# Kernel optimization log

Measured on AMD Instinct MI355X. Metric: run time of the kernel, lower is better.

The kernel has to match this reference:

```python
import jax, jax.numpy as jnp
import numpy as np

D_OUT = 1024

def setup_inputs() -> dict:
    key = jax.random.key(0)
    k1, k2, k3, k4 = jax.random.split(key, 4)
    x = jax.random.normal(k1, (4, 2048, 1024), dtype=jnp.float32)
    # torch.nn.Linear weights are [d_out, d_in]
    s = 1.0 / np.sqrt(1024)
    W_q = jax.random.uniform(k2, (D_OUT, 1024), dtype=jnp.float32, minval=-s, maxval=s)
    W_k = jax.random.uniform(k3, (D_OUT, 1024), dtype=jnp.float32, minval=-s, maxval=s)
    W_v = jax.random.uniform(k4, (D_OUT, 1024), dtype=jnp.float32, minval=-s, maxval=s)
    return {"x": x, "W_q": W_q, "W_k": W_k, "W_v": W_v}

def reference(x, W_q, W_k, W_v):
    b, n, d_in = x.shape
    q = jnp.einsum('bnd,od->bno', x, W_q)  # [b, n, d_out]
    k = jnp.einsum('bnd,od->bno', x, W_k)
    v = jnp.einsum('bnd,od->bno', x, W_v)
    scores = jnp.einsum('bqd,bkd->bqk', q, k)  # full N x N score matrix
    causal = jnp.tril(jnp.ones((n, n), dtype=bool))
    scores = jnp.where(causal, scores, -jnp.inf)
    weights = jax.nn.softmax(scores / jnp.sqrt(jnp.float32(D_OUT)), axis=-1)
    # dropout p=0.0 -> identity (eval)
    return jnp.einsum('bqk,bkd->bqd', weights, v)
```

## Files before the change

kernel.cpp:

```cpp
#include <hip/hip_runtime.h>
#include <hip/hip_bf16.h>
#include <stdint.h>
#include <math.h>

typedef unsigned short ushort_t;
typedef __attribute__((ext_vector_type(4))) float f32x4;
typedef __attribute__((ext_vector_type(8))) __bf16 bf16x8;
typedef __attribute__((ext_vector_type(8))) unsigned short ushort8;
typedef __attribute__((ext_vector_type(4))) unsigned short ushort4v;

__device__ __forceinline__ float bf2f(ushort_t u) {
  union { unsigned u32; float f; } x; x.u32 = ((unsigned)u) << 16; return x.f;
}
__device__ __forceinline__ ushort_t f2bf(float f) {
  union { float f; unsigned u; } x; x.f = f;
  unsigned r = x.u + 0x7FFF + ((x.u >> 16) & 1);
  return (ushort_t)(r >> 16);
}

__device__ __forceinline__ void gld16(const ushort_t* g, ushort_t* l) {
  __builtin_amdgcn_global_load_lds(
      (const __attribute__((address_space(1))) uint32_t*)g,
      (__attribute__((address_space(3))) uint32_t*)l, 16, 0, 0);
}

__global__ __launch_bounds__(256) void cast_all_kernel(
    const float* __restrict__ x, const float* __restrict__ wq,
    const float* __restrict__ wk, const float* __restrict__ wv,
    ushort_t* __restrict__ xb, ushort_t* __restrict__ wqb,
    ushort_t* __restrict__ wkb, ushort_t* __restrict__ wvb,
    float* __restrict__ rowsum) {
  int blk = blockIdx.x;
  if (blk >= 4096 + 1536) {
    int idx = (blk - (4096 + 1536)) * 256 + threadIdx.x;
    f32x4 z = {0.f, 0.f, 0.f, 0.f};
    ((f32x4*)rowsum)[idx * 2] = z;
    ((f32x4*)rowsum)[idx * 2 + 1] = z;
    return;
  }
  const float* in;
  ushort_t* out;
  int i;
  if (blk < 4096) {
    in = x; out = xb; i = blk * 256 + threadIdx.x;
  } else {
    int w = (blk - 4096) >> 9;
    int lb = (blk - 4096) & 511;
    in = (w == 0) ? wq : (w == 1) ? wk : wv;
    out = (w == 0) ? wqb : (w == 1) ? wkb : wvb;
    i = lb * 256 + threadIdx.x;
  }
  const f32x4* p = (const f32x4*)in;
  f32x4 a = p[2 * i];
  f32x4 b = p[2 * i + 1];
  ushort8 o;
  o[0] = f2bf(a[0]); o[1] = f2bf(a[1]); o[2] = f2bf(a[2]); o[3] = f2bf(a[3]);
  o[4] = f2bf(b[0]); o[5] = f2bf(b[1]); o[6] = f2bf(b[2]); o[7] = f2bf(b[3]);
  *((ushort8*)out + i) = o;
}

#define BM 128
#define BN 128
#define BK 64

__device__ __forceinline__ void gemm_core(
    const ushort_t* __restrict__ A, const ushort_t* __restrict__ B, int Kd,
    int kEnd, int m0, int n0, ushort_t* As, ushort_t* Bs, f32x4 (&acc)[4][4]) {
  int tid = threadIdx.x;
  int lane = tid & 63;
  int wave = tid >> 6;
  int wr = (wave >> 1) * 64;
  int wc = (wave & 1) * 64;
  int ln15 = lane & 15;
  int kq = lane >> 4;

  int row = tid >> 3;
  int ksw = ((tid & 7) ^ (row & 7)) * 8;
  const ushort_t* aB = A + (size_t)(m0 + row) * Kd + ksw;
  const ushort_t* bB = B + (size_t)(n0 + row) * Kd + ksw;
  int xk = ln15 & 7;

  for (int k0 = 0; k0 < kEnd; k0 += BK) {
    __syncthreads();
#pragma unroll
    for (int r = 0; r < 4; ++r) {
      gld16(aB + (size_t)(32 * r) * Kd + k0, &As[(tid + 256 * r) * 8]);
      gld16(bB + (size_t)(32 * r) * Kd + k0, &Bs[(tid + 256 * r) * 8]);
    }
    __syncthreads();
#pragma unroll
    for (int s = 0; s < 2; ++s) {
      bf16x8 af[4], bfr[4];
#pragma unroll
      for (int i = 0; i < 4; ++i)
        af[i] = *(const bf16x8*)
            &As[(wr + i * 16 + ln15) * BK + (((s * 4 + kq) ^ xk) * 8)];
#pragma unroll
      for (int j = 0; j < 4; ++j)
        bfr[j] = *(const bf16x8*)
            &Bs[(wc + j * 16 + ln15) * BK + (((s * 4 + kq) ^ xk) * 8)];
#pragma unroll
      for (int i = 0; i < 4; ++i)
#pragma unroll
        for (int j = 0; j < 4; ++j)
          acc[i][j] = __builtin_amdgcn_mfma_f32_16x16x32_bf16(
              af[i], bfr[j], acc[i][j], 0, 0, 0);
    }
  }
}

__global__ __launch_bounds__(256, 4) void gemm_s(
    const ushort_t* __restrict__ Qg, const ushort_t* __restrict__ Kg,
    ushort_t* __restrict__ Eg, float scale, float* __restrict__ rowsum) {
  int t = blockIdx.x;
  int m = (int)((sqrtf(8.f * (float)t + 1.f) - 1.f) * 0.5f);
  while ((m + 1) * (m + 2) / 2 <= t) ++m;
  while (m * (m + 1) / 2 > t) --m;
  int n = t - m * (m + 1) / 2;
  int m0 = m * BM, n0 = n * BN;
  int bz = blockIdx.z;
  const ushort_t* A = Qg + (size_t)bz * (2048 * 1024);
  const ushort_t* B = Kg + (size_t)bz * (2048 * 1024);

  __shared__ ushort_t As[BM * BK];
  __shared__ ushort_t Bs[BN * BK];

  f32x4 acc[4][4];
#pragma unroll
  for (int i = 0; i < 4; ++i)
#pragma unroll
    for (int j = 0; j < 4; ++j) acc[i][j] = f32x4{0.f, 0.f, 0.f, 0.f};

  gemm_core(A, B, 1024, 1024, m0, n0, As, Bs, acc);

  int tid = threadIdx.x;
  int lane = tid & 63;
  int wave = tid >> 6;
  int wr = (wave >> 1) * 64;
  int wc = (wave & 1) * 64;
  int ln15 = lane & 15;
  int kq = lane >> 4;

  ushort_t* C = Eg + (size_t)bz * (2048 * 2048);
  float* rs = rowsum + (size_t)bz * 2048;
#pragma unroll
  for (int i = 0; i < 4; ++i) {
    int row0 = m0 + wr + i * 16 + kq * 4;
#pragma unroll
    for (int r = 0; r < 4; ++r) {
      int grow = row0 + r;
      float psum = 0.f;
#pragma unroll
      for (int j = 0; j < 4; ++j) {
        int col = n0 + wc + j * 16 + ln15;
        float e = (col <= grow) ? __expf(acc[i][j][r] * scale) : 0.f;
        C[(size_t)grow * 2048 + col] = f2bf(e);
        psum += e;
      }
      psum += __shfl_xor(psum, 1);
      psum += __shfl_xor(psum, 2);
      psum += __shfl_xor(psum, 4);
      psum += __shfl_xor(psum, 8);
      if (ln15 == 0) atomicAdd(&rs[grow], psum);
    }
  }
}

__global__ __launch_bounds__(256, 4) void gemm_o(
    const ushort_t* __restrict__ Eg, const ushort_t* __restrict__ Vg,
    float* __restrict__ Og, const float* __restrict__ rowsum) {
  int m = (blockIdx.z < 2) ? (int)(gridDim.x - 1 - blockIdx.x)
                           : (int)blockIdx.x;
  int m0 = m * BM, n0 = blockIdx.y * BN;
  int kEnd = min(2048, m0 + BM);
  int bz = blockIdx.z;
  const ushort_t* A = Eg + (size_t)bz * (2048 * 2048);
  const ushort_t* B = Vg + (size_t)bz * (1024 * 2048);

  __shared__ ushort_t As[BM * BK];
  __shared__ ushort_t Bs[BN * BK];

  f32x4 acc[4][4];
#pragma unroll
  for (int i = 0; i < 4; ++i)
#pragma unroll
    for (int j = 0; j < 4; ++j) acc[i][j] = f32x4{0.f, 0.f, 0.f, 0.f};

  gemm_core(A, B, 2048, kEnd, m0, n0, As, Bs, acc);

  int tid = threadIdx.x;
  int lane = tid & 63;
  int wave = tid >> 6;
  int wr = (wave >> 1) * 64;
  int wc = (wave & 1) * 64;
  int ln15 = lane & 15;
  int kq = lane >> 4;

  float* C = Og + (size_t)bz * (2048 * 1024);
  const float* rs = rowsum + (size_t)bz * 2048;
#pragma unroll
  for (int i = 0; i < 4; ++i) {
    int row0 = m0 + wr + i * 16 + kq * 4;
#pragma unroll
    for (int r = 0; r < 4; ++r) {
      float inv = 1.0f / rs[row0 + r];
#pragma unroll
      for (int j = 0; j < 4; ++j) {
        int col = n0 + wc + j * 16 + ln15;
        C[(size_t)(row0 + r) * 1024 + col] = acc[i][j][r] * inv;
      }
    }
  }
}

__global__ __launch_bounds__(256, 4) void gemm_qkv(
    const ushort_t* __restrict__ xb, const ushort_t* __restrict__ wq,
    const ushort_t* __restrict__ wk, const ushort_t* __restrict__ wv,
    ushort_t* __restrict__ Qb, ushort_t* __restrict__ Kb,
    ushort_t* __restrict__ Vt) {
  int m0 = blockIdx.x * BM, n0 = blockIdx.y * BN;
  int z = blockIdx.z;
  const ushort_t* B = (z == 0) ? wq : (z == 1) ? wk : wv;

  __shared__ ushort_t As[BM * BK];
  __shared__ ushort_t Bs[BN * BK];

  f32x4 acc[4][4];
#pragma unroll
  for (int i = 0; i < 4; ++i)
#pragma unroll
    for (int j = 0; j < 4; ++j) acc[i][j] = f32x4{0.f, 0.f, 0.f, 0.f};

  gemm_core(xb, B, 1024, 1024, m0, n0, As, Bs, acc);

  int tid = threadIdx.x;
  int lane = tid & 63;
  int wave = tid >> 6;
  int wr = (wave >> 1) * 64;
  int wc = (wave & 1) * 64;
  int ln15 = lane & 15;
  int kq = lane >> 4;

  if (z < 2) {
    ushort_t* C = (z == 0) ? Qb : Kb;
#pragma unroll
    for (int i = 0; i < 4; ++i) {
      int row0 = m0 + wr + i * 16 + kq * 4;
#pragma unroll
      for (int j = 0; j < 4; ++j) {
        int col = n0 + wc + j * 16 + ln15;
#pragma unroll
        for (int r = 0; r < 4; ++r)
          C[(size_t)(row0 + r) * 1024 + col] = f2bf(acc[i][j][r]);
      }
    }
  } else {
#pragma unroll
    for (int i = 0; i < 4; ++i) {
      int gm = m0 + wr + i * 16 + kq * 4;
      int b = gm >> 11, nn = gm & 2047;
#pragma unroll
      for (int j = 0; j < 4; ++j) {
        int d = n0 + wc + j * 16 + ln15;
        ushort4v v;
#pragma unroll
        for (int r = 0; r < 4; ++r) v[r] = f2bf(acc[i][j][r]);
        *(ushort4v*)&Vt[(size_t)b * (2048 * 1024) + (size_t)d * 2048 + nn] = v;
      }
    }
  }
}

extern "C" void kernel_launch(void* const* d_in, const int* in_sizes, int n_in,
                              void* d_out, int out_size, void* d_ws, size_t ws_size,
                              hipStream_t stream) {
  const float* x = (const float*)d_in[0];
  const float* Wq = (const float*)d_in[1];
  const float* Wk = (const float*)d_in[2];
  const float* Wv = (const float*)d_in[3];
  float* out = (float*)d_out;
  char* ws = (char*)d_ws;

  ushort_t* xb = (ushort_t*)(ws);
  ushort_t* wqb = (ushort_t*)(ws + (16ull << 20));
  ushort_t* wkb = (ushort_t*)(ws + (18ull << 20));
  ushort_t* wvb = (ushort_t*)(ws + (20ull << 20));
  ushort_t* Qb = (ushort_t*)(ws + (22ull << 20));
  ushort_t* Kb = (ushort_t*)(ws + (38ull << 20));
  ushort_t* Vt = (ushort_t*)(ws + (54ull << 20));
  ushort_t* Eb = (ushort_t*)(ws + (70ull << 20));
  float* rowsum = (float*)(ws + (102ull << 20));

  cast_all_kernel<<<4096 + 3 * 512 + 4, 256, 0, stream>>>(
      x, Wq, Wk, Wv, xb, wqb, wkb, wvb, rowsum);

  dim3 gQKV(8192 / BM, 1024 / BN, 3);
  gemm_qkv<<<gQKV, 256, 0, stream>>>(xb, wqb, wkb, wvb, Qb, Kb, Vt);

  dim3 gS(136, 1, 4);
  gemm_s<<<gS, 256, 0, stream>>>(Qb, Kb, Eb, 0.03125f, rowsum);

  dim3 gO(2048 / BM, 1024 / BN, 4);
  gemm_o<<<gO, 256, 0, stream>>>(Eb, Vt, out, rowsum);
}
```

Measured before the change: 224.1 us.

## Rewrite QKV GEMM as 256x256 tile, 8-wave, double-buffered phased pipeline

Replaces the QKV projection GEMM with a 512-thread kernel that computes 256x256 output tiles. It uses double-buffered LDS and interleaves global-to-LDS loads across eight phases with explicit waitcnt, barriers and raised MFMA priority. The goal is to overlap memory traffic with MFMA work and cut global loads per flop through a larger tile. The launch-bounds occupancy hint for gemm_s and gemm_o also drops from 4 to 3 blocks, giving those kernels more registers at the cost of occupancy. The larger tile leaves only 384 blocks and needs 128 KB of LDS per block, and the hand-written vmcnt accounting is fragile.

```diff
diff --git a/kernel.cpp b/kernel.cpp
--- a/kernel.cpp
+++ b/kernel.cpp
@@ -109,7 +109,7 @@
   }
 }
 
-__global__ __launch_bounds__(256, 4) void gemm_s(
+__global__ __launch_bounds__(256, 3) void gemm_s(
     const ushort_t* __restrict__ Qg, const ushort_t* __restrict__ Kg,
     ushort_t* __restrict__ Eg, float scale, float* __restrict__ rowsum) {
   int t = blockIdx.x;
@@ -166,7 +166,7 @@
   }
 }
 
-__global__ __launch_bounds__(256, 4) void gemm_o(
+__global__ __launch_bounds__(256, 3) void gemm_o(
     const ushort_t* __restrict__ Eg, const ushort_t* __restrict__ Vg,
     float* __restrict__ Og, const float* __restrict__ rowsum) {
   int m = (blockIdx.z < 2) ? (int)(gridDim.x - 1 - blockIdx.x)
@@ -213,58 +213,118 @@
   }
 }
 
-__global__ __launch_bounds__(256, 4) void gemm_qkv(
+#define STA(BUF, T, Q) \
+  gld16(aS + (size_t)((Q) * 64) * 1024 + (T) * 64, &As[BUF][(Q)*4096 + tid * 8])
+#define STB(BUF, T, R) \
+  gld16(bS + (size_t)((R) * 64) * 1024 + (T) * 64, &Bs[BUF][(R)*4096 + tid * 8])
+
+#define PHASE(BUF, MH, KS, STAGES, TAIL) do {                               \
+    bf16x8 af[4], bfv[4];                                                   \
+    _Pragma("unroll")                                                       \
+    for (int f = 0; f < 4; ++f)                                             \
+      af[f] = *(const bf16x8*)&As[BUF][                                     \
+          (wm * 128 + (MH) * 64 + f * 16 + ln15) * 64 +                     \
+          ((((KS) * 4 + kq) ^ xk) * 8)];                                    \
+    _Pragma("unroll")                                                       \
+    for (int n = 0; n < 4; ++n)                                             \
+      bfv[n] = *(const bf16x8*)&Bs[BUF][                                    \
+          (wn * 64 + n * 16 + ln15) * 64 + ((((KS) * 4 + kq) ^ xk) * 8)];   \
+    STAGES;                                                                 \
+    asm volatile("s_waitcnt lgkmcnt(0)" ::: "memory");                      \
+    __builtin_amdgcn_sched_barrier(0);                                      \
+    __builtin_amdgcn_s_setprio(1);                                          \
+    _Pragma("unroll")                                                       \
+    for (int f = 0; f < 4; ++f)                                             \
+      _Pragma("unroll")                                                     \
+      for (int n = 0; n < 4; ++n)                                           \
+        acc[(MH) * 4 + f][n] = __builtin_amdgcn_mfma_f32_16x16x32_bf16(     \
+            af[f], bfv[n], acc[(MH) * 4 + f][n], 0, 0, 0);                  \
+    __builtin_amdgcn_s_setprio(0);                                          \
+    TAIL;                                                                   \
+    __builtin_amdgcn_sched_barrier(0);                                      \
+    __builtin_amdgcn_s_barrier();                                           \
+    __builtin_amdgcn_sched_barrier(0);                                      \
+  } while (0)
+
+__global__ __launch_bounds__(512, 2) void gemm_qkv8p(
     const ushort_t* __restrict__ xb, const ushort_t* __restrict__ wq,
     const ushort_t* __restrict__ wk, const ushort_t* __restrict__ wv,
     ushort_t* __restrict__ Qb, ushort_t* __restrict__ Kb,
     ushort_t* __restrict__ Vt) {
-  int m0 = blockIdx.x * BM, n0 = blockIdx.y * BN;
+  int m0 = blockIdx.x * 256, n0 = blockIdx.y * 256;
   int z = blockIdx.z;
-  const ushort_t* B = (z == 0) ? wq : (z == 1) ? wk : wv;
-
-  __shared__ ushort_t As[BM * BK];
-  __shared__ ushort_t Bs[BN * BK];
-
-  f32x4 acc[4][4];
-#pragma unroll
-  for (int i = 0; i < 4; ++i)
-#pragma unroll
-    for (int j = 0; j < 4; ++j) acc[i][j] = f32x4{0.f, 0.f, 0.f, 0.f};
-
-  gemm_core(xb, B, 1024, 1024, m0, n0, As, Bs, acc);
+  const ushort_t* Bw = (z == 0) ? wq : (z == 1) ? wk : wv;
+  const int nt = 16;
+
+  __shared__ ushort_t As[2][256 * 64];
+  __shared__ ushort_t Bs[2][256 * 64];
 
   int tid = threadIdx.x;
   int lane = tid & 63;
   int wave = tid >> 6;
-  int wr = (wave >> 1) * 64;
-  int wc = (wave & 1) * 64;
-  int ln15 = lane & 15;
-  int kq = lane >> 4;
+  int wm = wave >> 2, wn = wave & 3;
+  int ln15 = lane & 15, kq = lane >> 4, xk = ln15 & 7;
+
+  const ushort_t* aS = xb + (size_t)(m0 + (tid >> 3)) * 1024 +
+                       (((tid & 7) ^ ((tid >> 3) & 7)) * 8);
+  const ushort_t* bS = Bw + (size_t)(n0 + (tid >> 3)) * 1024 +
+                       (((tid & 7) ^ ((tid >> 3) & 7)) * 8);
+
+  f32x4 acc[8][4];
+#pragma unroll
+  for (int a = 0; a < 8; ++a)
+#pragma unroll
+    for (int n = 0; n < 4; ++n) acc[a][n] = f32x4{0.f, 0.f, 0.f, 0.f};
+
+  STA(0, 0, 0); STA(0, 0, 1); STA(0, 0, 2); STA(0, 0, 3);
+  STB(0, 0, 0); STB(0, 0, 1); STB(0, 0, 2); STB(0, 0, 3);
+  STA(1, 1, 0); STA(1, 1, 2);
+  asm volatile("s_waitcnt vmcnt(2)" ::: "memory");
+  __builtin_amdgcn_sched_barrier(0);
+  __builtin_amdgcn_s_barrier();
+  __builtin_amdgcn_sched_barrier(0);
+
+  for (int i = 0; i < nt / 2; ++i) {
+    int t0 = 2 * i, t1 = 2 * i + 1;
+    bool s2 = (t0 + 2) < nt, s3 = (t1 + 2) < nt;
+    PHASE(0, 0, 0,
+          { STA(1, t1, 1); STA(1, t1, 3); STB(1, t1, 0); STB(1, t1, 1); }, );
+    PHASE(0, 0, 1, { STB(1, t1, 2); STB(1, t1, 3); }, );
+    PHASE(0, 1, 0, { if (s2) { STA(0, t0 + 2, 0); STA(0, t0 + 2, 2); } }, );
+    PHASE(0, 1, 1, , {
+      if (s2) { asm volatile("s_waitcnt vmcnt(2)" ::: "memory"); }
+      else    { asm volatile("s_waitcnt vmcnt(0)" ::: "memory"); } });
+    PHASE(1, 0, 0, { if (s2) { STA(0, t0 + 2, 1); STA(0, t0 + 2, 3); } }, );
+    PHASE(1, 0, 1, { if (s2) { STB(0, t0 + 2, 0); STB(0, t0 + 2, 1); } }, );
+    PHASE(1, 1, 0, { if (s2) { STB(0, t0 + 2, 2); STB(0, t0 + 2, 3); } }, );
+    PHASE(1, 1, 1, { if (s3) { STA(1, t1 + 2, 0); STA(1, t1 + 2, 2); } },
+          { asm volatile("s_waitcnt vmcnt(2)" ::: "memory"); });
+  }
 
   if (z < 2) {
     ushort_t* C = (z == 0) ? Qb : Kb;
 #pragma unroll
-    for (int i = 0; i < 4; ++i) {
-      int row0 = m0 + wr + i * 16 + kq * 4;
-#pragma unroll
-      for (int j = 0; j < 4; ++j) {
-        int col = n0 + wc + j * 16 + ln15;
+    for (int a = 0; a < 8; ++a) {
+      int row0 = m0 + wm * 128 + (a >> 2) * 64 + (a & 3) * 16 + kq * 4;
+#pragma unroll
+      for (int n = 0; n < 4; ++n) {
+        int col = n0 + wn * 64 + n * 16 + ln15;
 #pragma unroll
         for (int r = 0; r < 4; ++r)
-          C[(size_t)(row0 + r) * 1024 + col] = f2bf(acc[i][j][r]);
+          C[(size_t)(row0 + r) * 1024 + col] = f2bf(acc[a][n][r]);
       }
     }
   } else {
 #pragma unroll
-    for (int i = 0; i < 4; ++i) {
-      int gm = m0 + wr + i * 16 + kq * 4;
+    for (int a = 0; a < 8; ++a) {
+      int gm = m0 + wm * 128 + (a >> 2) * 64 + (a & 3) * 16 + kq * 4;
       int b = gm >> 11, nn = gm & 2047;
 #pragma unroll
-      for (int j = 0; j < 4; ++j) {
-        int d = n0 + wc + j * 16 + ln15;
+      for (int n = 0; n < 4; ++n) {
+        int d = n0 + wn * 64 + n * 16 + ln15;
         ushort4v v;
 #pragma unroll
-        for (int r = 0; r < 4; ++r) v[r] = f2bf(acc[i][j][r]);
+        for (int r = 0; r < 4; ++r) v[r] = f2bf(acc[a][n][r]);
         *(ushort4v*)&Vt[(size_t)b * (2048 * 1024) + (size_t)d * 2048 + nn] = v;
       }
     }
@@ -294,8 +354,8 @@
   cast_all_kernel<<<4096 + 3 * 512 + 4, 256, 0, stream>>>(
       x, Wq, Wk, Wv, xb, wqb, wkb, wvb, rowsum);
 
-  dim3 gQKV(8192 / BM, 1024 / BN, 3);
-  gemm_qkv<<<gQKV, 256, 0, stream>>>(xb, wqb, wkb, wvb, Qb, Kb, Vt);
+  dim3 gQKV(8192 / 256, 1024 / 256, 3);
+  gemm_qkv8p<<<gQKV, 512, 0, stream>>>(xb, wqb, wkb, wvb, Qb, Kb, Vt);
 
   dim3 gS(136, 1, 4);
   gemm_s<<<gS, 256, 0, stream>>>(Qb, Kb, Eb, 0.03125f, rowsum);
```

Measured after the change: 239.0 us. +6.6%, slower.

## Move V projection into the score kernel launch to balance work

Applied to the files above, without the earlier changes.

The QKV projection kernel now computes only Q and K. The V projection tiles are appended to the causal score kernel's grid, so one launch handles both the triangular S tiles and the V GEMM tiles. The aim is to fill the idle tail of the triangular score grid with independent V work, while the QK launch shrinks. Launch bounds are also lowered from 4 to 3 blocks per CU, which permits more registers per thread but lowers occupancy.

```diff
diff --git a/kernel.cpp b/kernel.cpp
--- a/kernel.cpp
+++ b/kernel.cpp
@@ -109,18 +109,13 @@
   }
 }
 
-__global__ __launch_bounds__(256, 4) void gemm_s(
-    const ushort_t* __restrict__ Qg, const ushort_t* __restrict__ Kg,
-    ushort_t* __restrict__ Eg, float scale, float* __restrict__ rowsum) {
-  int t = blockIdx.x;
-  int m = (int)((sqrtf(8.f * (float)t + 1.f) - 1.f) * 0.5f);
-  while ((m + 1) * (m + 2) / 2 <= t) ++m;
-  while (m * (m + 1) / 2 > t) --m;
-  int n = t - m * (m + 1) / 2;
-  int m0 = m * BM, n0 = n * BN;
-  int bz = blockIdx.z;
-  const ushort_t* A = Qg + (size_t)bz * (2048 * 1024);
-  const ushort_t* B = Kg + (size_t)bz * (2048 * 1024);
+__global__ __launch_bounds__(256, 3) void gemm_qk(
+    const ushort_t* __restrict__ xb, const ushort_t* __restrict__ wq,
+    const ushort_t* __restrict__ wk, ushort_t* __restrict__ Qb,
+    ushort_t* __restrict__ Kb) {
+  int m0 = blockIdx.x * BM, n0 = blockIdx.y * BN;
+  int z = blockIdx.z;
+  const ushort_t* B = (z == 0) ? wq : wk;
 
   __shared__ ushort_t As[BM * BK];
   __shared__ ushort_t Bs[BN * BK];
@@ -131,7 +126,7 @@
 #pragma unroll
     for (int j = 0; j < 4; ++j) acc[i][j] = f32x4{0.f, 0.f, 0.f, 0.f};
 
-  gemm_core(A, B, 1024, 1024, m0, n0, As, Bs, acc);
+  gemm_core(xb, B, 1024, 1024, m0, n0, As, Bs, acc);
 
   int tid = threadIdx.x;
   int lane = tid & 63;
@@ -141,32 +136,108 @@
   int ln15 = lane & 15;
   int kq = lane >> 4;
 
-  ushort_t* C = Eg + (size_t)bz * (2048 * 2048);
-  float* rs = rowsum + (size_t)bz * 2048;
+  ushort_t* C = (z == 0) ? Qb : Kb;
 #pragma unroll
   for (int i = 0; i < 4; ++i) {
     int row0 = m0 + wr + i * 16 + kq * 4;
 #pragma unroll
-    for (int r = 0; r < 4; ++r) {
-      int grow = row0 + r;
-      float psum = 0.f;
+    for (int j = 0; j < 4; ++j) {
+      int col = n0 + wc + j * 16 + ln15;
+#pragma unroll
+      for (int r = 0; r < 4; ++r)
+        C[(size_t)(row0 + r) * 1024 + col] = f2bf(acc[i][j][r]);
+    }
+  }
+}
+
+__global__ __launch_bounds__(256, 3) void gemm_sv(
+    const ushort_t* __restrict__ Qg, const ushort_t* __restrict__ Kg,
+    const ushort_t* __restrict__ xb, const ushort_t* __restrict__ wv,
+    ushort_t* __restrict__ Eg, ushort_t* __restrict__ Vt,
+    float scale, float* __restrict__ rowsum) {
+  int bx = blockIdx.x;
+  int bz = blockIdx.z;
+  bool isS = bx < 136;
+  int m0, n0;
+  const ushort_t *A, *B;
+  if (isS) {
+    int t = bx;
+    int m = (int)((sqrtf(8.f * (float)t + 1.f) - 1.f) * 0.5f);
+    while ((m + 1) * (m + 2) / 2 <= t) ++m;
+    while (m * (m + 1) / 2 > t) --m;
+    int n = t - m * (m + 1) / 2;
+    m0 = m * BM; n0 = n * BN;
+    A = Qg + (size_t)bz * (2048 * 1024);
+    B = Kg + (size_t)bz * (2048 * 1024);
+  } else {
+    int vid = (bx - 136) + 128 * bz;
+    m0 = (vid >> 3) * BM;
+    n0 = (vid & 7) * BN;
+    A = xb;
+    B = wv;
+  }
+
+  __shared__ ushort_t As[BM * BK];
+  __shared__ ushort_t Bs[BN * BK];
+
+  f32x4 acc[4][4];
+#pragma unroll
+  for (int i = 0; i < 4; ++i)
+#pragma unroll
+    for (int j = 0; j < 4; ++j) acc[i][j] = f32x4{0.f, 0.f, 0.f, 0.f};
+
+  gemm_core(A, B, 1024, 1024, m0, n0, As, Bs, acc);
+
+  int tid = threadIdx.x;
+  int lane = tid & 63;
+  int wave = tid >> 6;
+  int wr = (wave >> 1) * 64;
+  int wc = (wave & 1) * 64;
+  int ln15 = lane & 15;
+  int kq = lane >> 4;
+
+  if (isS) {
+    ushort_t* C = Eg + (size_t)bz * (2048 * 2048);
+    float* rs = rowsum + (size_t)bz * 2048;
+#pragma unroll
+    for (int i = 0; i < 4; ++i) {
+      int row0 = m0 + wr + i * 16 + kq * 4;
+#pragma unroll
+      for (int r = 0; r < 4; ++r) {
+        int grow = row0 + r;
+        float psum = 0.f;
+#pragma unroll
+        for (int j = 0; j < 4; ++j) {
+          int col = n0 + wc + j * 16 + ln15;
+          float e = (col <= grow) ? __expf(acc[i][j][r] * scale) : 0.f;
+          C[(size_t)grow * 2048 + col] = f2bf(e);
+          psum += e;
+        }
+        psum += __shfl_xor(psum, 1);
+        psum += __shfl_xor(psum, 2);
+        psum += __shfl_xor(psum, 4);
+        psum += __shfl_xor(psum, 8);
+        if (ln15 == 0) atomicAdd(&rs[grow], psum);
+      }
+    }
+  } else {
+#pragma unroll
+    for (int i = 0; i < 4; ++i) {
+      int gm = m0 + wr + i * 16 + kq * 4;
+      int b = gm >> 11, nn = gm & 2047;
 #pragma unroll
       for (int j = 0; j < 4; ++j) {
-        int col = n0 + wc + j * 16 + ln15;
-        float e = (col <= grow) ? __expf(acc[i][j][r] * scale) : 0.f;
-        C[(size_t)grow * 2048 + col] = f2bf(e);
-        psum += e;
+        int d = n0 + wc + j * 16 + ln15;
+        ushort4v v;
+#pragma unroll
+        for (int r = 0; r < 4; ++r) v[r] = f2bf(acc[i][j][r]);
+        *(ushort4v*)&Vt[(size_t)b * (2048 * 1024) + (size_t)d * 2048 + nn] = v;
       }
-      psum += __shfl_xor(psum, 1);
-      psum += __shfl_xor(psum, 2);
-      psum += __shfl_xor(psum, 4);
-      psum += __shfl_xor(psum, 8);
-      if (ln15 == 0) atomicAdd(&rs[grow], psum);
-    }
-  }
-}
-
-__global__ __launch_bounds__(256, 4) void gemm_o(
+    }
+  }
+}
+
+__global__ __launch_bounds__(256, 3) void gemm_o(
     const ushort_t* __restrict__ Eg, const ushort_t* __restrict__ Vg,
     float* __restrict__ Og, const float* __restrict__ rowsum) {
   int m = (blockIdx.z < 2) ? (int)(gridDim.x - 1 - blockIdx.x)
@@ -213,64 +284,6 @@
   }
 }
 
-__global__ __launch_bounds__(256, 4) void gemm_qkv(
-    const ushort_t* __restrict__ xb, const ushort_t* __restrict__ wq,
-    const ushort_t* __restrict__ wk, const ushort_t* __restrict__ wv,
-    ushort_t* __restrict__ Qb, ushort_t* __restrict__ Kb,
-    ushort_t* __restrict__ Vt) {
-  int m0 = blockIdx.x * BM, n0 = blockIdx.y * BN;
-  int z = blockIdx.z;
-  const ushort_t* B = (z == 0) ? wq : (z == 1) ? wk : wv;
-
-  __shared__ ushort_t As[BM * BK];
-  __shared__ ushort_t Bs[BN * BK];
-
-  f32x4 acc[4][4];
-#pragma unroll
-  for (int i = 0; i < 4; ++i)
-#pragma unroll
-    for (int j = 0; j < 4; ++j) acc[i][j] = f32x4{0.f, 0.f, 0.f, 0.f};
-
-  gemm_core(xb, B, 1024, 1024, m0, n0, As, Bs, acc);
-
-  int tid = threadIdx.x;
-  int lane = tid & 63;
-  int wave = tid >> 6;
-  int wr = (wave >> 1) * 64;
-  int wc = (wave & 1) * 64;
-  int ln15 = lane & 15;
-  int kq = lane >> 4;
-
-  if (z < 2) {
-    ushort_t* C = (z == 0) ? Qb : Kb;
-#pragma unroll
-    for (int i = 0; i < 4; ++i) {
-      int row0 = m0 + wr + i * 16 + kq * 4;
-#pragma unroll
-      for (int j = 0; j < 4; ++j) {
-        int col = n0 + wc + j * 16 + ln15;
-#pragma unroll
-        for (int r = 0; r < 4; ++r)
-          C[(size_t)(row0 + r) * 1024 + col] = f2bf(acc[i][j][r]);
-      }
-    }
-  } else {
-#pragma unroll
-    for (int i = 0; i < 4; ++i) {
-      int gm = m0 + wr + i * 16 + kq * 4;
-      int b = gm >> 11, nn = gm & 2047;
-#pragma unroll
-      for (int j = 0; j < 4; ++j) {
-        int d = n0 + wc + j * 16 + ln15;
-        ushort4v v;
-#pragma unroll
-        for (int r = 0; r < 4; ++r) v[r] = f2bf(acc[i][j][r]);
-        *(ushort4v*)&Vt[(size_t)b * (2048 * 1024) + (size_t)d * 2048 + nn] = v;
-      }
-    }
-  }
-}
-
 extern "C" void kernel_launch(void* const* d_in, const int* in_sizes, int n_in,
                               void* d_out, int out_size, void* d_ws, size_t ws_size,
                               hipStream_t stream) {
@@ -294,11 +307,11 @@
   cast_all_kernel<<<4096 + 3 * 512 + 4, 256, 0, stream>>>(
       x, Wq, Wk, Wv, xb, wqb, wkb, wvb, rowsum);
 
-  dim3 gQKV(8192 / BM, 1024 / BN, 3);
-  gemm_qkv<<<gQKV, 256, 0, stream>>>(xb, wqb, wkb, wvb, Qb, Kb, Vt);
-
-  dim3 gS(136, 1, 4);
-  gemm_s<<<gS, 256, 0, stream>>>(Qb, Kb, Eb, 0.03125f, rowsum);
+  dim3 gQK(8192 / BM, 1024 / BN, 2);
+  gemm_qk<<<gQK, 256, 0, stream>>>(xb, wqb, wkb, Qb, Kb);
+
+  dim3 gSV(136 + 128, 1, 4);
+  gemm_sv<<<gSV, 256, 0, stream>>>(Qb, Kb, xb, wvb, Eb, Vt, 0.03125f, rowsum);
 
   dim3 gO(2048 / BM, 1024 / BN, 4);
   gemm_o<<<gO, 256, 0, stream>>>(Eb, Vt, out, rowsum);
```

Result: no change. 222.9 us (-0.6%).

## Remap GEMM block indices to XCDs so each batch stays in one L2

Applied to the files above, without the earlier changes.

Flattens all three GEMM grids to 1D and decodes the block index so blocks dispatched round-robin to the same XCD work on the same batch (two XCDs per batch), keeping Q/K/V/E reuse inside one XCD's L2. The causal score tiles are split between the XCD pair with a balancing rule, and the output GEMM interleaves long and short row-tiles. Launch bounds also drop from 4 to 3 waves per SIMD. This relies on the hardware's round-robin dispatch order across XCDs, and the serial tile-search loop in gemm_s adds a little per-block overhead.

```diff
diff --git a/kernel.cpp b/kernel.cpp
--- a/kernel.cpp
+++ b/kernel.cpp
@@ -109,18 +109,22 @@
   }
 }
 
-__global__ __launch_bounds__(256, 4) void gemm_s(
-    const ushort_t* __restrict__ Qg, const ushort_t* __restrict__ Kg,
-    ushort_t* __restrict__ Eg, float scale, float* __restrict__ rowsum) {
-  int t = blockIdx.x;
-  int m = (int)((sqrtf(8.f * (float)t + 1.f) - 1.f) * 0.5f);
-  while ((m + 1) * (m + 2) / 2 <= t) ++m;
-  while (m * (m + 1) / 2 > t) --m;
-  int n = t - m * (m + 1) / 2;
-  int m0 = m * BM, n0 = n * BN;
-  int bz = blockIdx.z;
-  const ushort_t* A = Qg + (size_t)bz * (2048 * 1024);
-  const ushort_t* B = Kg + (size_t)bz * (2048 * 1024);
+__global__ __launch_bounds__(256, 3) void gemm_qkv(
+    const ushort_t* __restrict__ xb, const ushort_t* __restrict__ wq,
+    const ushort_t* __restrict__ wk, const ushort_t* __restrict__ wv,
+    ushort_t* __restrict__ Qb, ushort_t* __restrict__ Kb,
+    ushort_t* __restrict__ Vt) {
+  int L = blockIdx.x;
+  int xcd = L & 7;
+  int slot = L >> 3;
+  int bz = xcd >> 1, p = xcd & 1;
+  int zz = slot >> 6;
+  int tt = slot & 63;
+  int m_local = ((tt >> 3) << 1) + p;
+  int n = tt & 7;
+  int m0 = (bz * 16 + m_local) * BM;
+  int n0 = n * BN;
+  const ushort_t* B = (zz == 0) ? wq : (zz == 1) ? wk : wv;
 
   __shared__ ushort_t As[BM * BK];
   __shared__ ushort_t Bs[BN * BK];
@@ -131,7 +135,7 @@
 #pragma unroll
     for (int j = 0; j < 4; ++j) acc[i][j] = f32x4{0.f, 0.f, 0.f, 0.f};
 
-  gemm_core(A, B, 1024, 1024, m0, n0, As, Bs, acc);
+  gemm_core(xb, B, 1024, 1024, m0, n0, As, Bs, acc);
 
   int tid = threadIdx.x;
   int lane = tid & 63;
@@ -141,41 +145,55 @@
   int ln15 = lane & 15;
   int kq = lane >> 4;
 
-  ushort_t* C = Eg + (size_t)bz * (2048 * 2048);
-  float* rs = rowsum + (size_t)bz * 2048;
-#pragma unroll
-  for (int i = 0; i < 4; ++i) {
-    int row0 = m0 + wr + i * 16 + kq * 4;
-#pragma unroll
-    for (int r = 0; r < 4; ++r) {
-      int grow = row0 + r;
-      float psum = 0.f;
+  if (zz < 2) {
+    ushort_t* C = (zz == 0) ? Qb : Kb;
+#pragma unroll
+    for (int i = 0; i < 4; ++i) {
+      int row0 = m0 + wr + i * 16 + kq * 4;
 #pragma unroll
       for (int j = 0; j < 4; ++j) {
         int col = n0 + wc + j * 16 + ln15;
-        float e = (col <= grow) ? __expf(acc[i][j][r] * scale) : 0.f;
-        C[(size_t)grow * 2048 + col] = f2bf(e);
-        psum += e;
-      }
-      psum += __shfl_xor(psum, 1);
-      psum += __shfl_xor(psum, 2);
-      psum += __shfl_xor(psum, 4);
-      psum += __shfl_xor(psum, 8);
-      if (ln15 == 0) atomicAdd(&rs[grow], psum);
-    }
-  }
-}
-
-__global__ __launch_bounds__(256, 4) void gemm_o(
-    const ushort_t* __restrict__ Eg, const ushort_t* __restrict__ Vg,
-    float* __restrict__ Og, const float* __restrict__ rowsum) {
-  int m = (blockIdx.z < 2) ? (int)(gridDim.x - 1 - blockIdx.x)
-                           : (int)blockIdx.x;
-  int m0 = m * BM, n0 = blockIdx.y * BN;
-  int kEnd = min(2048, m0 + BM);
-  int bz = blockIdx.z;
-  const ushort_t* A = Eg + (size_t)bz * (2048 * 2048);
-  const ushort_t* B = Vg + (size_t)bz * (1024 * 2048);
+#pragma unroll
+        for (int r = 0; r < 4; ++r)
+          C[(size_t)(row0 + r) * 1024 + col] = f2bf(acc[i][j][r]);
+      }
+    }
+  } else {
+#pragma unroll
+    for (int i = 0; i < 4; ++i) {
+      int gm = m0 + wr + i * 16 + kq * 4;
+      int b = gm >> 11, nn = gm & 2047;
+#pragma unroll
+      for (int j = 0; j < 4; ++j) {
+        int d = n0 + wc + j * 16 + ln15;
+        ushort4v v;
+#pragma unroll
+        for (int r = 0; r < 4; ++r) v[r] = f2bf(acc[i][j][r]);
+        *(ushort4v*)&Vt[(size_t)b * (2048 * 1024) + (size_t)d * 2048 + nn] = v;
+      }
+    }
+  }
+}
+
+__global__ __launch_bounds__(256, 3) void gemm_s(
+    const ushort_t* __restrict__ Qg, const ushort_t* __restrict__ Kg,
+    ushort_t* __restrict__ Eg, float scale, float* __restrict__ rowsum) {
+  int L = blockIdx.x;
+  int xcd = L & 7;
+  int slot = L >> 3;
+  int bz = xcd >> 1, p = xcd & 1;
+  int t = slot, m = 16, n = 0;
+  for (int mi = 0; mi < 16 && m == 16; ++mi)
+    for (int ni = 0; ni <= mi; ++ni) {
+      int assignOdd = (ni & 1) || ((ni == mi) && !(ni & 1) && (mi >= 8));
+      if (assignOdd == p) {
+        if (t == 0) { m = mi; n = ni; break; }
+        --t;
+      }
+    }
+  int m0 = m * BM, n0 = n * BN;
+  const ushort_t* A = Qg + (size_t)bz * (2048 * 1024);
+  const ushort_t* B = Kg + (size_t)bz * (2048 * 1024);
 
   __shared__ ushort_t As[BM * BK];
   __shared__ ushort_t Bs[BN * BK];
@@ -186,7 +204,7 @@
 #pragma unroll
     for (int j = 0; j < 4; ++j) acc[i][j] = f32x4{0.f, 0.f, 0.f, 0.f};
 
-  gemm_core(A, B, 2048, kEnd, m0, n0, As, Bs, acc);
+  gemm_core(A, B, 1024, 1024, m0, n0, As, Bs, acc);
 
   int tid = threadIdx.x;
   int lane = tid & 63;
@@ -196,31 +214,46 @@
   int ln15 = lane & 15;
   int kq = lane >> 4;
 
-  float* C = Og + (size_t)bz * (2048 * 1024);
-  const float* rs = rowsum + (size_t)bz * 2048;
+  ushort_t* C = Eg + (size_t)bz * (2048 * 2048);
+  float* rs = rowsum + (size_t)bz * 2048;
 #pragma unroll
   for (int i = 0; i < 4; ++i) {
     int row0 = m0 + wr + i * 16 + kq * 4;
 #pragma unroll
     for (int r = 0; r < 4; ++r) {
-      float inv = 1.0f / rs[row0 + r];
+      int grow = row0 + r;
+      float psum = 0.f;
 #pragma unroll
       for (int j = 0; j < 4; ++j) {
         int col = n0 + wc + j * 16 + ln15;
-        C[(size_t)(row0 + r) * 1024 + col] = acc[i][j][r] * inv;
-      }
-    }
-  }
-}
-
-__global__ __launch_bounds__(256, 4) void gemm_qkv(
-    const ushort_t* __restrict__ xb, const ushort_t* __restrict__ wq,
-    const ushort_t* __restrict__ wk, const ushort_t* __restrict__ wv,
-    ushort_t* __restrict__ Qb, ushort_t* __restrict__ Kb,
-    ushort_t* __restrict__ Vt) {
-  int m0 = blockIdx.x * BM, n0 = blockIdx.y * BN;
-  int z = blockIdx.z;
-  const ushort_t* B = (z == 0) ? wq : (z == 1) ? wk : wv;
+        float e = (col <= grow) ? __expf(acc[i][j][r] * scale) : 0.f;
+        C[(size_t)grow * 2048 + col] = f2bf(e);
+        psum += e;
+      }
+      psum += __shfl_xor(psum, 1);
+      psum += __shfl_xor(psum, 2);
+      psum += __shfl_xor(psum, 4);
+      psum += __shfl_xor(psum, 8);
+      if (ln15 == 0) atomicAdd(&rs[grow], psum);
+    }
+  }
+}
+
+__global__ __launch_bounds__(256, 3) void gemm_o(
+    const ushort_t* __restrict__ Eg, const ushort_t* __restrict__ Vg,
+    float* __restrict__ Og, const float* __restrict__ rowsum) {
+  int L = blockIdx.x;
+  int xcd = L & 7;
+  int slot = L >> 3;
+  int bz = xcd >> 1;
+  int idx = ((xcd & 1) * 64) + slot;
+  int n = idx & 7;
+  int mm = idx >> 3;
+  int m = (mm & 1) ? (mm >> 1) : (15 - (mm >> 1));
+  int m0 = m * BM, n0 = n * BN;
+  int kEnd = min(2048, m0 + BM);
+  const ushort_t* A = Eg + (size_t)bz * (2048 * 2048);
+  const ushort_t* B = Vg + (size_t)bz * (1024 * 2048);
 
   __shared__ ushort_t As[BM * BK];
   __shared__ ushort_t Bs[BN * BK];
@@ -231,7 +264,7 @@
 #pragma unroll
     for (int j = 0; j < 4; ++j) acc[i][j] = f32x4{0.f, 0.f, 0.f, 0.f};
 
-  gemm_core(xb, B, 1024, 1024, m0, n0, As, Bs, acc);
+  gemm_core(A, B, 2048, kEnd, m0, n0, As, Bs, acc);
 
   int tid = threadIdx.x;
   int lane = tid & 63;
@@ -241,31 +274,18 @@
   int ln15 = lane & 15;
   int kq = lane >> 4;
 
-  if (z < 2) {
-    ushort_t* C = (z == 0) ? Qb : Kb;
-#pragma unroll
-    for (int i = 0; i < 4; ++i) {
-      int row0 = m0 + wr + i * 16 + kq * 4;
+  float* C = Og + (size_t)bz * (2048 * 1024);
+  const float* rs = rowsum + (size_t)bz * 2048;
+#pragma unroll
+  for (int i = 0; i < 4; ++i) {
+    int row0 = m0 + wr + i * 16 + kq * 4;
+#pragma unroll
+    for (int r = 0; r < 4; ++r) {
+      float inv = 1.0f / rs[row0 + r];
 #pragma unroll
       for (int j = 0; j < 4; ++j) {
         int col = n0 + wc + j * 16 + ln15;
-#pragma unroll
-        for (int r = 0; r < 4; ++r)
-          C[(size_t)(row0 + r) * 1024 + col] = f2bf(acc[i][j][r]);
-      }
-    }
-  } else {
-#pragma unroll
-    for (int i = 0; i < 4; ++i) {
-      int gm = m0 + wr + i * 16 + kq * 4;
-      int b = gm >> 11, nn = gm & 2047;
-#pragma unroll
-      for (int j = 0; j < 4; ++j) {
-        int d = n0 + wc + j * 16 + ln15;
-        ushort4v v;
-#pragma unroll
-        for (int r = 0; r < 4; ++r) v[r] = f2bf(acc[i][j][r]);
-        *(ushort4v*)&Vt[(size_t)b * (2048 * 1024) + (size_t)d * 2048 + nn] = v;
+        C[(size_t)(row0 + r) * 1024 + col] = acc[i][j][r] * inv;
       }
     }
   }
@@ -294,12 +314,10 @@
   cast_all_kernel<<<4096 + 3 * 512 + 4, 256, 0, stream>>>(
       x, Wq, Wk, Wv, xb, wqb, wkb, wvb, rowsum);
 
-  dim3 gQKV(8192 / BM, 1024 / BN, 3);
-  gemm_qkv<<<gQKV, 256, 0, stream>>>(xb, wqb, wkb, wvb, Qb, Kb, Vt);
-
-  dim3 gS(136, 1, 4);
-  gemm_s<<<gS, 256, 0, stream>>>(Qb, Kb, Eb, 0.03125f, rowsum);
-
-  dim3 gO(2048 / BM, 1024 / BN, 4);
-  gemm_o<<<gO, 256, 0, stream>>>(Eb, Vt, out, rowsum);
-}
+  gemm_qkv<<<dim3(1536, 1, 1), 256, 0, stream>>>(
+      xb, wqb, wkb, wvb, Qb, Kb, Vt);
+
+  gemm_s<<<dim3(544, 1, 1), 256, 0, stream>>>(Qb, Kb, Eb, 0.03125f, rowsum);
+
+  gemm_o<<<dim3(512, 1, 1), 256, 0, stream>>>(Eb, Vt, out, rowsum);
+}
```

Result: faster. 216.3 us (-3.5%).
